# Kernel tuning notes

Hardware: AMD Instinct MI355X
Metric: run time of the kernel (lower is better)

## Reference

```python
import jax, jax.numpy as jnp
import numpy as np

N = 100000      # nodes
E = 1_000_000   # edges (avg degree ~10)
D_IN = 64
HID = 64
N_CLS = 32


def setup_inputs() -> dict:
    key = jax.random.key(0)
    ks = jax.random.split(key, 9)
    x = jax.random.normal(ks[0], (N, D_IN), dtype=jnp.float32)
    edge_index = jax.random.randint(ks[1], (2, E), 0, N, dtype=jnp.int32)
    s_in = 1.0 / np.sqrt(D_IN)
    s_h = 1.0 / np.sqrt(HID)
    W1 = jax.random.normal(ks[2], (D_IN, HID), dtype=jnp.float32) * s_in
    b1 = jnp.zeros((HID,), dtype=jnp.float32)
    W2 = jax.random.normal(ks[3], (HID, HID), dtype=jnp.float32) * s_h
    b2 = jnp.zeros((HID,), dtype=jnp.float32)
    Wl = jax.random.normal(ks[4], (HID, N_CLS), dtype=jnp.float32) * s_h
    bl = jnp.zeros((N_CLS,), dtype=jnp.float32)
    return {"x": x, "edge_index": edge_index,
            "W1": W1, "b1": b1, "W2": W2, "b2": b2, "Wl": Wl, "bl": bl}


def reference(x, edge_index, W1, b1, W2, b2, Wl, bl):
    # GCNConv default: add self-loops, symmetric normalization D^-1/2 (A+I) D^-1/2
    loop = jnp.arange(N, dtype=edge_index.dtype)
    src = jnp.concatenate([edge_index[0], loop])  # [E+N]
    dst = jnp.concatenate([edge_index[1], loop])  # [E+N]

    deg = jax.ops.segment_sum(jnp.ones_like(dst, dtype=jnp.float32), dst,
                              num_segments=N)              # [N]
    dinv = jnp.where(deg > 0, jax.lax.rsqrt(deg), 0.0)      # D^-1/2
    norm = dinv[src] * dinv[dst]                            # [E+N]

    def gcn_conv(h, W, b):
        h = h @ W                                           # [N, F_out]
        msg = h[src] * norm[:, None]                        # gather + scale
        return jax.ops.segment_sum(msg, dst, num_segments=N) + b

    h = jax.nn.relu(gcn_conv(x, W1, b1))
    h = jax.nn.relu(gcn_conv(h, W2, b2))
    return h @ Wl + bl
```

## Files before the change

### kernel.cpp

```cpp
#include <hip/hip_runtime.h>
#include <hip/hip_fp16.h>
#include <math.h>


#define TPB    256
#define TPB1   1024
#define EBLKS  256
#define BSH    7
#define BNODES (1 << BSH)

__global__ __launch_bounds__(TPB1)
void k_p1hist(const int* __restrict__ dst, int* __restrict__ OFS,
              int E, int CH, int NBC) {
    __shared__ int h[1024];
    int tid = threadIdx.x, b = blockIdx.x;
    h[tid] = 0;
    __syncthreads();
    int beg = b * CH, end = min(E, beg + CH);
    if (beg < end) {
        int nfull = (end - beg) & ~3;
        for (int i = beg + tid * 4; i < beg + nfull; i += TPB1 * 4) {
            int4 d = *(const int4*)&dst[i];
            atomicAdd(&h[d.x >> BSH], 1);
            atomicAdd(&h[d.y >> BSH], 1);
            atomicAdd(&h[d.z >> BSH], 1);
            atomicAdd(&h[d.w >> BSH], 1);
        }
        if (tid < (end - beg) - nfull)
            atomicAdd(&h[dst[beg + nfull + tid] >> BSH], 1);
    }
    __syncthreads();
    for (int c = tid; c < NBC; c += TPB1) OFS[c * EBLKS + b] = h[c];
}

__global__ __launch_bounds__(TPB)
void k_scanA(const int* __restrict__ OFS, int* __restrict__ bsum, int total) {
    __shared__ int s[TPB];
    int tid = threadIdx.x;
    int i0  = blockIdx.x * 1024 + tid * 4;
    int t = 0;
#pragma unroll
    for (int k = 0; k < 4; ++k) {
        int i = i0 + k;
        t += (i < total) ? OFS[i] : 0;
    }
    s[tid] = t;
    __syncthreads();
    for (int off = TPB / 2; off > 0; off >>= 1) {
        if (tid < off) s[tid] += s[tid + off];
        __syncthreads();
    }
    if (tid == 0) bsum[blockIdx.x] = s[0];
}

__global__ __launch_bounds__(TPB)
void k_scanC(int* __restrict__ OFS, const int* __restrict__ bsum, int total) {
    __shared__ int s[TPB];
    __shared__ int pfx;
    int tid = threadIdx.x;
    if (tid < 64) {
        int v = 0;
        for (int j = tid; j < (int)blockIdx.x; j += 64) v += bsum[j];
#pragma unroll
        for (int off = 1; off < 64; off <<= 1) v += __shfl_xor(v, off);
        if (tid == 0) pfx = v;
    }
    int i0 = blockIdx.x * 1024 + tid * 4;
    int v[4];
#pragma unroll
    for (int k = 0; k < 4; ++k) {
        int i = i0 + k;
        v[k] = (i < total) ? OFS[i] : 0;
    }
    int tsum = v[0] + v[1] + v[2] + v[3];
    s[tid] = tsum;
    __syncthreads();
    for (int off = 1; off < TPB; off <<= 1) {
        int x = (tid >= off) ? s[tid - off] : 0;
        __syncthreads();
        s[tid] += x;
        __syncthreads();
    }
    int base = pfx + (s[tid] - tsum);
#pragma unroll
    for (int k = 0; k < 4; ++k) {
        int i = i0 + k;
        if (i < total) {
            OFS[i] = base;
            base += v[k];
        }
    }
}

__global__ __launch_bounds__(TPB1)
void k_p1scatter(const int* __restrict__ src, const int* __restrict__ dst,
                 const int* __restrict__ OFS, int* __restrict__ ebuf,
                 int E, int CH, int NBC) {
    __shared__ int cur[1024];
    int tid = threadIdx.x, b = blockIdx.x;
    for (int c = tid; c < NBC; c += TPB1) cur[c] = OFS[c * EBLKS + b];
    __syncthreads();
    int beg = b * CH, end = min(E, beg + CH);
    if (beg >= end) return;
    int nfull = (end - beg) & ~3;
    for (int i = beg + tid * 4; i < beg + nfull; i += TPB1 * 4) {
        int4 s4 = *(const int4*)&src[i];
        int4 d4 = *(const int4*)&dst[i];
        int p0 = atomicAdd(&cur[d4.x >> BSH], 1);
        int p1 = atomicAdd(&cur[d4.y >> BSH], 1);
        int p2 = atomicAdd(&cur[d4.z >> BSH], 1);
        int p3 = atomicAdd(&cur[d4.w >> BSH], 1);
        ebuf[p0] = (s4.x << BSH) | (d4.x & (BNODES - 1));
        ebuf[p1] = (s4.y << BSH) | (d4.y & (BNODES - 1));
        ebuf[p2] = (s4.z << BSH) | (d4.z & (BNODES - 1));
        ebuf[p3] = (s4.w << BSH) | (d4.w & (BNODES - 1));
    }
    if (tid < (end - beg) - nfull) {
        int i = beg + nfull + tid;
        int d = dst[i];
        int p = atomicAdd(&cur[d >> BSH], 1);
        ebuf[p] = (src[i] << BSH) | (d & (BNODES - 1));
    }
}

__global__ __launch_bounds__(TPB)
void k_p2(const int* __restrict__ ebuf, const int* __restrict__ OFS,
          int* __restrict__ row_ptr, float* __restrict__ dinv,
          int* __restrict__ colw, int N, int E, int NBC) {
    __shared__ int cnt[BNODES];
    __shared__ int ofs[BNODES];
    __shared__ int s1[TPB];
    int tid = threadIdx.x, c = blockIdx.x;
    int beg = OFS[c * EBLKS];
    int end = (c == NBC - 1) ? E : OFS[(c + 1) * EBLKS];
    if (tid < BNODES) cnt[tid] = 0;
    __syncthreads();
    for (int i = beg + tid; i < end; i += TPB)
        atomicAdd(&cnt[ebuf[i] & (BNODES - 1)], 1);
    __syncthreads();
    int a = (tid < BNODES) ? cnt[tid] : 0;
    s1[tid] = a;
    __syncthreads();
    for (int off = 1; off < TPB; off <<= 1) {
        int x = (tid >= off) ? s1[tid - off] : 0;
        __syncthreads();
        s1[tid] += x;
        __syncthreads();
    }
    int ex = s1[tid] - a;
    if (tid < BNODES) {
        int node = (c << BSH) + tid;
        ofs[tid] = beg + ex;
        if (node < N) {
            row_ptr[node] = beg + ex;
            dinv[node]    = rsqrtf((float)(a + 1));
        }
        cnt[tid] = 0;
    }
    if (c == NBC - 1 && tid == 0) row_ptr[N] = E;
    __syncthreads();
    for (int i0 = beg + tid; i0 < end; i0 += TPB * 4) {
        int sv[4], dl[4], pos[4];
        int have = 0;
#pragma unroll
        for (int k = 0; k < 4; ++k) {
            int i = i0 + k * TPB;
            if (i < end) {
                int e = ebuf[i];
                sv[k] = e >> BSH;
                dl[k] = e & (BNODES - 1);
                have = k + 1;
            }
        }
#pragma unroll
        for (int k = 0; k < 4; ++k) {
            if (k < have) {
                int r  = atomicAdd(&cnt[dl[k]], 1);
                pos[k] = ofs[dl[k]] + r;
            }
        }
#pragma unroll
        for (int k = 0; k < 4; ++k)
            if (k < have) colw[pos[k]] = sv[k];
    }
}

__launch_bounds__(256)
__global__ void k_mm(const float* __restrict__ in, const float* __restrict__ W,
                     const float* __restrict__ dinv,
                     __half* __restrict__ out, int n) {
    __shared__ float in_s[64 * 68];
    __shared__ float w_s[64 * 64];

    const int tid  = threadIdx.x;
    const int row0 = blockIdx.x * 64;

    for (int i4 = tid; i4 < (64 * 64) / 4; i4 += 256)
        ((float4*)w_s)[i4] = ((const float4*)W)[i4];

    for (int idx = tid; idx < 64 * 16; idx += 256) {
        int r  = idx >> 4;
        int c4 = idx & 15;
        float4 v;
        if (row0 + r < n)
            v = *(const float4*)(in + (size_t)(row0 + r) * 64 + c4 * 4);
        else
            v = make_float4(0.f, 0.f, 0.f, 0.f);
        *(float4*)&in_s[r * 68 + c4 * 4] = v;
    }
    __syncthreads();

    constexpr int CPT = 4;
    const int tx = tid & 15;
    const int ty = tid >> 4;

    float acc[4][CPT];
#pragma unroll
    for (int r = 0; r < 4; ++r)
#pragma unroll
        for (int c = 0; c < CPT; ++c) acc[r][c] = 0.f;

#pragma unroll 4
    for (int k = 0; k < 64; ++k) {
        float b[CPT];
#pragma unroll
        for (int c = 0; c < CPT; ++c) b[c] = w_s[k * 64 + tx * CPT + c];
#pragma unroll
        for (int r = 0; r < 4; ++r) {
            float a = in_s[(ty * 4 + r) * 68 + k];
#pragma unroll
            for (int c = 0; c < CPT; ++c) acc[r][c] = fmaf(a, b[c], acc[r][c]);
        }
    }

#pragma unroll
    for (int r = 0; r < 4; ++r) {
        int row = row0 + ty * 4 + r;
        if (row >= n) continue;
        float dd = dinv[row];
        __half2 p0 = __floats2half2_rn(acc[r][0] * dd, acc[r][1] * dd);
        __half2 p1 = __floats2half2_rn(acc[r][2] * dd, acc[r][3] * dd);
        uint2 u = make_uint2(*(unsigned*)&p0, *(unsigned*)&p1);
        *(uint2*)(out + (size_t)row * 64 + tx * 4) = u;
    }
    if (blockIdx.x == 0 && tid < 16)
        *(uint2*)(out + (size_t)n * 64 + tid * 4) = make_uint2(0u, 0u);
}

__global__ __launch_bounds__(256)
void k_gather_mm(const int* __restrict__ row_ptr, const int* __restrict__ colw,
                 const float* __restrict__ dinv, const float* __restrict__ bias,
                 const __half* __restrict__ t, const float* __restrict__ W2,
                 __half* __restrict__ t2, int N) {
    __shared__ float  w_s[64 * 64];
    __shared__ __half aggs[32][72];

    int tid = threadIdx.x;
    for (int i4 = tid; i4 < (64 * 64) / 4; i4 += 256)
        ((float4*)w_s)[i4] = ((const float4*)W2)[i4];

    int wv   = tid >> 6;
    int lane = tid & 63;
    int g = lane >> 3;
    int p = lane & 7;
    int slot = tid >> 3;
    int d = blockIdx.x * 32 + wv * 8 + g;

    int beg = 0, end = 0;
    if (d < N) { beg = row_ptr[d]; end = row_ptr[d + 1]; }

    float acc[8];
#pragma unroll
    for (int k = 0; k < 8; ++k) acc[k] = 0.f;

    for (int e = beg; e < end; e += 4) {
        int s0 = colw[e];
        int s1 = (e + 1 < end) ? colw[e + 1] : N;
        int s2 = (e + 2 < end) ? colw[e + 2] : N;
        int s3 = (e + 3 < end) ? colw[e + 3] : N;
        uint4 a0 = *(const uint4*)(t + (size_t)s0 * 64 + p * 8);
        uint4 a1 = *(const uint4*)(t + (size_t)s1 * 64 + p * 8);
        uint4 a2 = *(const uint4*)(t + (size_t)s2 * 64 + p * 8);
        uint4 a3 = *(const uint4*)(t + (size_t)s3 * 64 + p * 8);
        float2 f;
        f = __half22float2(*(__half2*)&a0.x); acc[0] += f.x; acc[1] += f.y;
        f = __half22float2(*(__half2*)&a0.y); acc[2] += f.x; acc[3] += f.y;
        f = __half22float2(*(__half2*)&a0.z); acc[4] += f.x; acc[5] += f.y;
        f = __half22float2(*(__half2*)&a0.w); acc[6] += f.x; acc[7] += f.y;
        f = __half22float2(*(__half2*)&a1.x); acc[0] += f.x; acc[1] += f.y;
        f = __half22float2(*(__half2*)&a1.y); acc[2] += f.x; acc[3] += f.y;
        f = __half22float2(*(__half2*)&a1.z); acc[4] += f.x; acc[5] += f.y;
        f = __half22float2(*(__half2*)&a1.w); acc[6] += f.x; acc[7] += f.y;
        f = __half22float2(*(__half2*)&a2.x); acc[0] += f.x; acc[1] += f.y;
        f = __half22float2(*(__half2*)&a2.y); acc[2] += f.x; acc[3] += f.y;
        f = __half22float2(*(__half2*)&a2.z); acc[4] += f.x; acc[5] += f.y;
        f = __half22float2(*(__half2*)&a2.w); acc[6] += f.x; acc[7] += f.y;
        f = __half22float2(*(__half2*)&a3.x); acc[0] += f.x; acc[1] += f.y;
        f = __half22float2(*(__half2*)&a3.y); acc[2] += f.x; acc[3] += f.y;
        f = __half22float2(*(__half2*)&a3.z); acc[4] += f.x; acc[5] += f.y;
        f = __half22float2(*(__half2*)&a3.w); acc[6] += f.x; acc[7] += f.y;
    }

    if (d < N) {
        float dd = dinv[d];
        uint4 a = *(const uint4*)(t + (size_t)d * 64 + p * 8);
        float4 b0 = *(const float4*)&bias[p * 8];
        float4 b1 = *(const float4*)&bias[p * 8 + 4];
        float2 s0 = __half22float2(*(__half2*)&a.x);
        float2 s1 = __half22float2(*(__half2*)&a.y);
        float2 s2 = __half22float2(*(__half2*)&a.z);
        float2 s3 = __half22float2(*(__half2*)&a.w);
        float o0 = fmaxf(fmaf(dd, acc[0] + s0.x, b0.x), 0.f);
        float o1 = fmaxf(fmaf(dd, acc[1] + s0.y, b0.y), 0.f);
        float o2 = fmaxf(fmaf(dd, acc[2] + s1.x, b0.z), 0.f);
        float o3 = fmaxf(fmaf(dd, acc[3] + s1.y, b0.w), 0.f);
        float o4 = fmaxf(fmaf(dd, acc[4] + s2.x, b1.x), 0.f);
        float o5 = fmaxf(fmaf(dd, acc[5] + s2.y, b1.y), 0.f);
        float o6 = fmaxf(fmaf(dd, acc[6] + s3.x, b1.z), 0.f);
        float o7 = fmaxf(fmaf(dd, acc[7] + s3.y, b1.w), 0.f);
        __half2 h0 = __floats2half2_rn(o0, o1);
        __half2 h1 = __floats2half2_rn(o2, o3);
        __half2 h2 = __floats2half2_rn(o4, o5);
        __half2 h3 = __floats2half2_rn(o6, o7);
        *(uint4*)&aggs[slot][p * 8] = make_uint4(*(unsigned*)&h0, *(unsigned*)&h1,
                                                *(unsigned*)&h2, *(unsigned*)&h3);
    }
    __syncthreads();

    if (d < N) {
        float dd = dinv[d];
        float a0 = 0.f, a1 = 0.f, a2 = 0.f, a3 = 0.f;
        float a4 = 0.f, a5 = 0.f, a6 = 0.f, a7 = 0.f;
#pragma unroll
        for (int k0 = 0; k0 < 64; k0 += 8) {
            uint4 u = *(const uint4*)&aggs[slot][k0];
            float2 f0 = __half22float2(*(__half2*)&u.x);
            float2 f1 = __half22float2(*(__half2*)&u.y);
            float2 f2 = __half22float2(*(__half2*)&u.z);
            float2 f3 = __half22float2(*(__half2*)&u.w);
            float av[8] = {f0.x, f0.y, f1.x, f1.y, f2.x, f2.y, f3.x, f3.y};
#pragma unroll
            for (int j = 0; j < 8; ++j) {
                const float* wr = &w_s[(k0 + j) * 64 + p * 8];
                float4 w0 = *(const float4*)&wr[0];
                float4 w1 = *(const float4*)&wr[4];
                a0 = fmaf(av[j], w0.x, a0);
                a1 = fmaf(av[j], w0.y, a1);
                a2 = fmaf(av[j], w0.z, a2);
                a3 = fmaf(av[j], w0.w, a3);
                a4 = fmaf(av[j], w1.x, a4);
                a5 = fmaf(av[j], w1.y, a5);
                a6 = fmaf(av[j], w1.z, a6);
                a7 = fmaf(av[j], w1.w, a7);
            }
        }
        __half2 q0 = __floats2half2_rn(a0 * dd, a1 * dd);
        __half2 q1 = __floats2half2_rn(a2 * dd, a3 * dd);
        __half2 q2 = __floats2half2_rn(a4 * dd, a5 * dd);
        __half2 q3 = __floats2half2_rn(a6 * dd, a7 * dd);
        uint4 u = make_uint4(*(unsigned*)&q0, *(unsigned*)&q1,
                             *(unsigned*)&q2, *(unsigned*)&q3);
        *(uint4*)(t2 + (size_t)d * 64 + p * 8) = u;
    }
    if (blockIdx.x == 0 && tid < 16)
        *(uint2*)(t2 + (size_t)N * 64 + tid * 4) = make_uint2(0u, 0u);
}

__global__ __launch_bounds__(256)
void k_gather_head(const int* __restrict__ row_ptr, const int* __restrict__ colw,
                   const float* __restrict__ dinv, const float* __restrict__ bias,
                   const __half* __restrict__ t, const float* __restrict__ Wl,
                   const float* __restrict__ bl, float* __restrict__ out, int N) {
    __shared__ float wl_s[64 * 32];
    __shared__ float aggs[32][68];

    int tid  = threadIdx.x;
    for (int i4 = tid; i4 < (64 * 32) / 4; i4 += 256)
        ((float4*)wl_s)[i4] = ((const float4*)Wl)[i4];

    int wv   = tid >> 6;
    int lane = tid & 63;
    int g = lane >> 3;
    int p = lane & 7;
    int slot = tid >> 3;
    int d = blockIdx.x * 32 + wv * 8 + g;

    int beg = 0, end = 0;
    if (d < N) { beg = row_ptr[d]; end = row_ptr[d + 1]; }

    float acc[8];
#pragma unroll
    for (int k = 0; k < 8; ++k) acc[k] = 0.f;

    for (int e = beg; e < end; e += 4) {
        int s0 = colw[e];
        int s1 = (e + 1 < end) ? colw[e + 1] : N;
        int s2 = (e + 2 < end) ? colw[e + 2] : N;
        int s3 = (e + 3 < end) ? colw[e + 3] : N;
        uint4 a0 = *(const uint4*)(t + (size_t)s0 * 64 + p * 8);
        uint4 a1 = *(const uint4*)(t + (size_t)s1 * 64 + p * 8);
        uint4 a2 = *(const uint4*)(t + (size_t)s2 * 64 + p * 8);
        uint4 a3 = *(const uint4*)(t + (size_t)s3 * 64 + p * 8);
        float2 f;
        f = __half22float2(*(__half2*)&a0.x); acc[0] += f.x; acc[1] += f.y;
        f = __half22float2(*(__half2*)&a0.y); acc[2] += f.x; acc[3] += f.y;
        f = __half22float2(*(__half2*)&a0.z); acc[4] += f.x; acc[5] += f.y;
        f = __half22float2(*(__half2*)&a0.w); acc[6] += f.x; acc[7] += f.y;
        f = __half22float2(*(__half2*)&a1.x); acc[0] += f.x; acc[1] += f.y;
        f = __half22float2(*(__half2*)&a1.y); acc[2] += f.x; acc[3] += f.y;
        f = __half22float2(*(__half2*)&a1.z); acc[4] += f.x; acc[5] += f.y;
        f = __half22float2(*(__half2*)&a1.w); acc[6] += f.x; acc[7] += f.y;
        f = __half22float2(*(__half2*)&a2.x); acc[0] += f.x; acc[1] += f.y;
        f = __half22float2(*(__half2*)&a2.y); acc[2] += f.x; acc[3] += f.y;
        f = __half22float2(*(__half2*)&a2.z); acc[4] += f.x; acc[5] += f.y;
        f = __half22float2(*(__half2*)&a2.w); acc[6] += f.x; acc[7] += f.y;
        f = __half22float2(*(__half2*)&a3.x); acc[0] += f.x; acc[1] += f.y;
        f = __half22float2(*(__half2*)&a3.y); acc[2] += f.x; acc[3] += f.y;
        f = __half22float2(*(__half2*)&a3.z); acc[4] += f.x; acc[5] += f.y;
        f = __half22float2(*(__half2*)&a3.w); acc[6] += f.x; acc[7] += f.y;
    }

    if (d < N) {
        float dd = dinv[d];
        uint4 a = *(const uint4*)(t + (size_t)d * 64 + p * 8);
        float4 b0 = *(const float4*)&bias[p * 8];
        float4 b1 = *(const float4*)&bias[p * 8 + 4];
        float2 s0 = __half22float2(*(__half2*)&a.x);
        float2 s1 = __half22float2(*(__half2*)&a.y);
        float2 s2 = __half22float2(*(__half2*)&a.z);
        float2 s3 = __half22float2(*(__half2*)&a.w);
        float o0 = fmaxf(fmaf(dd, acc[0] + s0.x, b0.x), 0.f);
        float o1 = fmaxf(fmaf(dd, acc[1] + s0.y, b0.y), 0.f);
        float o2 = fmaxf(fmaf(dd, acc[2] + s1.x, b0.z), 0.f);
        float o3 = fmaxf(fmaf(dd, acc[3] + s1.y, b0.w), 0.f);
        float o4 = fmaxf(fmaf(dd, acc[4] + s2.x, b1.x), 0.f);
        float o5 = fmaxf(fmaf(dd, acc[5] + s2.y, b1.y), 0.f);
        float o6 = fmaxf(fmaf(dd, acc[6] + s3.x, b1.z), 0.f);
        float o7 = fmaxf(fmaf(dd, acc[7] + s3.y, b1.w), 0.f);
        *(float4*)&aggs[slot][p * 8]     = make_float4(o0, o1, o2, o3);
        *(float4*)&aggs[slot][p * 8 + 4] = make_float4(o4, o5, o6, o7);
    }
    __syncthreads();

    if (d < N) {
        float a0 = 0.f, a1 = 0.f, a2 = 0.f, a3 = 0.f;
#pragma unroll 8
        for (int k = 0; k < 64; ++k) {
            float av = aggs[slot][k];
            float4 w = ((const float4*)&wl_s[k * 32])[p];
            a0 = fmaf(av, w.x, a0);
            a1 = fmaf(av, w.y, a1);
            a2 = fmaf(av, w.z, a2);
            a3 = fmaf(av, w.w, a3);
        }
        float4 bb = *(const float4*)&bl[p * 4];
        *(float4*)&out[(size_t)d * 32 + p * 4] =
            make_float4(a0 + bb.x, a1 + bb.y, a2 + bb.z, a3 + bb.w);
    }
}

extern "C" void kernel_launch(void* const* d_in, const int* in_sizes, int n_in,
                              void* d_out, int out_size, void* d_ws, size_t ws_size,
                              hipStream_t stream) {
    const float* x  = (const float*)d_in[0];
    const int*   ei = (const int*)d_in[1];
    const float* W1 = (const float*)d_in[2];
    const float* b1 = (const float*)d_in[3];
    const float* W2 = (const float*)d_in[4];
    const float* b2 = (const float*)d_in[5];
    const float* Wl = (const float*)d_in[6];
    const float* bl = (const float*)d_in[7];
    float*       out = (float*)d_out;

    const int N = in_sizes[0] / 64;
    const int E = in_sizes[1] / 2;
    const int* srcp = ei;
    const int* dstp = ei + E;

    const int NBC   = (N + BNODES - 1) / BNODES;
    const int CH    = (((E + EBLKS - 1) / EBLKS) + 3) & ~3;
    const int total = NBC * EBLKS;
    const int NBLK  = (total + 1023) / 1024;

    char*  ws  = (char*)d_ws;
    size_t off = 0;
    auto alloc = [&](size_t bytes) -> void* {
        void* p = (void*)(ws + off);
        off += (bytes + 255) & ~(size_t)255;
        return p;
    };
    int*    OFS     = (int*)alloc(((size_t)total + 1) * 4);
    int*    bsum    = (int*)alloc((size_t)NBLK * 4);
    int*    ebuf    = (int*)alloc((size_t)E * 4);
    int*    row_ptr = (int*)alloc((size_t)(N + 1) * 4);
    float*  dinv    = (float*)alloc((size_t)N * 4);
    int*    colw    = (int*)alloc((size_t)E * 4);
    __half* t1      = (__half*)alloc((size_t)(N + 1) * 64 * 2);
    __half* t2      = (__half*)alloc((size_t)(N + 1) * 64 * 2);

    const int nb_mm = (N + 63) / 64;
    const int nb_g  = (N + 31) / 32;

    k_p1hist   <<<EBLKS, TPB1, 0, stream>>>(dstp, OFS, E, CH, NBC);
    k_scanA    <<<NBLK,  TPB,  0, stream>>>(OFS, bsum, total);
    k_scanC    <<<NBLK,  TPB,  0, stream>>>(OFS, bsum, total);
    k_p1scatter<<<EBLKS, TPB1, 0, stream>>>(srcp, dstp, OFS, ebuf, E, CH, NBC);
    k_p2       <<<NBC,   TPB,  0, stream>>>(ebuf, OFS, row_ptr, dinv, colw, N, E, NBC);

    k_mm<<<nb_mm, 256, 0, stream>>>(x, W1, dinv, t1, N);

    k_gather_mm<<<nb_g, 256, 0, stream>>>(row_ptr, colw, dinv, b1, t1,
                                          W2, t2, N);

    k_gather_head<<<nb_g, 256, 0, stream>>>(row_ptr, colw, dinv, b2, t2,
                                            Wl, bl, out, N);
}
```

Before: 187.1 us.

## Fuse scan into single pass and merge CSR build with first matmul

The two-kernel scan (block sums, then prefix) is replaced by one kernel in which each block re-reads and sums all preceding OFS entries itself, writing to a separate OFS2 buffer to avoid read/write races. The per-bucket CSR build kernel now also performs the x@W1 matmul for its 128 nodes, using the dinv values it already holds in shared memory. This removes two kernel launches and a global dinv re-read. In exchange the scan does redundant reads that grow with block index, and the fused kernel uses more shared memory, which may lower occupancy.

```diff
diff --git a/kernel.cpp b/kernel.cpp
--- a/kernel.cpp
+++ b/kernel.cpp
@@ -34,38 +34,27 @@
 }
 
 __global__ __launch_bounds__(TPB)
-void k_scanA(const int* __restrict__ OFS, int* __restrict__ bsum, int total) {
+void k_scan1(const int* __restrict__ OFS, int* __restrict__ OFS2, int total) {
     __shared__ int s[TPB];
+    __shared__ int pfxs;
     int tid = threadIdx.x;
-    int i0  = blockIdx.x * 1024 + tid * 4;
-    int t = 0;
-#pragma unroll
-    for (int k = 0; k < 4; ++k) {
-        int i = i0 + k;
-        t += (i < total) ? OFS[i] : 0;
-    }
-    s[tid] = t;
+    int lim = blockIdx.x * 1024;
+
+    int acc = 0;
+    for (int i = tid * 4; i < lim; i += TPB * 4) {
+        int4 v = *(const int4*)&OFS[i];
+        acc += v.x + v.y + v.z + v.w;
+    }
+    s[tid] = acc;
     __syncthreads();
     for (int off = TPB / 2; off > 0; off >>= 1) {
         if (tid < off) s[tid] += s[tid + off];
         __syncthreads();
     }
-    if (tid == 0) bsum[blockIdx.x] = s[0];
-}
-
-__global__ __launch_bounds__(TPB)
-void k_scanC(int* __restrict__ OFS, const int* __restrict__ bsum, int total) {
-    __shared__ int s[TPB];
-    __shared__ int pfx;
-    int tid = threadIdx.x;
-    if (tid < 64) {
-        int v = 0;
-        for (int j = tid; j < (int)blockIdx.x; j += 64) v += bsum[j];
-#pragma unroll
-        for (int off = 1; off < 64; off <<= 1) v += __shfl_xor(v, off);
-        if (tid == 0) pfx = v;
-    }
-    int i0 = blockIdx.x * 1024 + tid * 4;
+    if (tid == 0) pfxs = s[0];
+    __syncthreads();
+
+    int i0 = lim + tid * 4;
     int v[4];
 #pragma unroll
     for (int k = 0; k < 4; ++k) {
@@ -81,12 +70,12 @@
         s[tid] += x;
         __syncthreads();
     }
-    int base = pfx + (s[tid] - tsum);
+    int base = pfxs + (s[tid] - tsum);
 #pragma unroll
     for (int k = 0; k < 4; ++k) {
         int i = i0 + k;
         if (i < total) {
-            OFS[i] = base;
+            OFS2[i] = base;
             base += v[k];
         }
     }
@@ -94,11 +83,11 @@
 
 __global__ __launch_bounds__(TPB1)
 void k_p1scatter(const int* __restrict__ src, const int* __restrict__ dst,
-                 const int* __restrict__ OFS, int* __restrict__ ebuf,
+                 const int* __restrict__ OFS2, int* __restrict__ ebuf,
                  int E, int CH, int NBC) {
     __shared__ int cur[1024];
     int tid = threadIdx.x, b = blockIdx.x;
-    for (int c = tid; c < NBC; c += TPB1) cur[c] = OFS[c * EBLKS + b];
+    for (int c = tid; c < NBC; c += TPB1) cur[c] = OFS2[c * EBLKS + b];
     __syncthreads();
     int beg = b * CH, end = min(E, beg + CH);
     if (beg >= end) return;
@@ -124,15 +113,25 @@
 }
 
 __global__ __launch_bounds__(TPB)
-void k_p2(const int* __restrict__ ebuf, const int* __restrict__ OFS,
-          int* __restrict__ row_ptr, float* __restrict__ dinv,
-          int* __restrict__ colw, int N, int E, int NBC) {
-    __shared__ int cnt[BNODES];
-    __shared__ int ofs[BNODES];
-    __shared__ int s1[TPB];
+void k_p2mm(const int* __restrict__ ebuf, const int* __restrict__ OFS2,
+            const float* __restrict__ x, const float* __restrict__ W1,
+            int* __restrict__ row_ptr, float* __restrict__ dinv,
+            int* __restrict__ colw, __half* __restrict__ t1,
+            int N, int E, int NBC) {
+    __shared__ int   cnt[BNODES];
+    __shared__ int   ofs[BNODES];
+    __shared__ int   s1[TPB];
+    __shared__ float dinv_s[BNODES];
+    __shared__ float in_s[64 * 68];
+    __shared__ float w_s[64 * 64];
+
     int tid = threadIdx.x, c = blockIdx.x;
-    int beg = OFS[c * EBLKS];
-    int end = (c == NBC - 1) ? E : OFS[(c + 1) * EBLKS];
+
+    for (int i4 = tid; i4 < (64 * 64) / 4; i4 += TPB)
+        ((float4*)w_s)[i4] = ((const float4*)W1)[i4];
+
+    int beg = OFS2[c * EBLKS];
+    int end = (c == NBC - 1) ? E : OFS2[(c + 1) * EBLKS];
     if (tid < BNODES) cnt[tid] = 0;
     __syncthreads();
     for (int i = beg + tid; i < end; i += TPB)
@@ -142,18 +141,20 @@
     s1[tid] = a;
     __syncthreads();
     for (int off = 1; off < TPB; off <<= 1) {
-        int x = (tid >= off) ? s1[tid - off] : 0;
-        __syncthreads();
-        s1[tid] += x;
+        int v = (tid >= off) ? s1[tid - off] : 0;
+        __syncthreads();
+        s1[tid] += v;
         __syncthreads();
     }
     int ex = s1[tid] - a;
     if (tid < BNODES) {
         int node = (c << BSH) + tid;
-        ofs[tid] = beg + ex;
+        float dv = rsqrtf((float)(a + 1));
+        ofs[tid]    = beg + ex;
+        dinv_s[tid] = dv;
         if (node < N) {
             row_ptr[node] = beg + ex;
-            dinv[node]    = rsqrtf((float)(a + 1));
+            dinv[node]    = dv;
         }
         cnt[tid] = 0;
     }
@@ -183,68 +184,57 @@
         for (int k = 0; k < 4; ++k)
             if (k < have) colw[pos[k]] = sv[k];
     }
-}
-
-__launch_bounds__(256)
-__global__ void k_mm(const float* __restrict__ in, const float* __restrict__ W,
-                     const float* __restrict__ dinv,
-                     __half* __restrict__ out, int n) {
-    __shared__ float in_s[64 * 68];
-    __shared__ float w_s[64 * 64];
-
-    const int tid  = threadIdx.x;
-    const int row0 = blockIdx.x * 64;
-
-    for (int i4 = tid; i4 < (64 * 64) / 4; i4 += 256)
-        ((float4*)w_s)[i4] = ((const float4*)W)[i4];
-
-    for (int idx = tid; idx < 64 * 16; idx += 256) {
-        int r  = idx >> 4;
-        int c4 = idx & 15;
-        float4 v;
-        if (row0 + r < n)
-            v = *(const float4*)(in + (size_t)(row0 + r) * 64 + c4 * 4);
-        else
-            v = make_float4(0.f, 0.f, 0.f, 0.f);
-        *(float4*)&in_s[r * 68 + c4 * 4] = v;
-    }
-    __syncthreads();
-
-    constexpr int CPT = 4;
+
     const int tx = tid & 15;
     const int ty = tid >> 4;
-
-    float acc[4][CPT];
-#pragma unroll
-    for (int r = 0; r < 4; ++r)
-#pragma unroll
-        for (int c = 0; c < CPT; ++c) acc[r][c] = 0.f;
+#pragma unroll
+    for (int half = 0; half < 2; ++half) {
+        const int row0 = (c << BSH) + half * 64;
+        __syncthreads();
+        for (int idx = tid; idx < 64 * 16; idx += TPB) {
+            int r  = idx >> 4;
+            int c4 = idx & 15;
+            float4 v = make_float4(0.f, 0.f, 0.f, 0.f);
+            if (row0 + r < N)
+                v = *(const float4*)(x + (size_t)(row0 + r) * 64 + c4 * 4);
+            *(float4*)&in_s[r * 68 + c4 * 4] = v;
+        }
+        __syncthreads();
+
+        float acc[4][4];
+#pragma unroll
+        for (int r = 0; r < 4; ++r)
+#pragma unroll
+            for (int cc = 0; cc < 4; ++cc) acc[r][cc] = 0.f;
 
 #pragma unroll 4
-    for (int k = 0; k < 64; ++k) {
-        float b[CPT];
-#pragma unroll
-        for (int c = 0; c < CPT; ++c) b[c] = w_s[k * 64 + tx * CPT + c];
+        for (int k = 0; k < 64; ++k) {
+            float b[4];
+#pragma unroll
+            for (int cc = 0; cc < 4; ++cc) b[cc] = w_s[k * 64 + tx * 4 + cc];
+#pragma unroll
+            for (int r = 0; r < 4; ++r) {
+                float av = in_s[(ty * 4 + r) * 68 + k];
+#pragma unroll
+                for (int cc = 0; cc < 4; ++cc)
+                    acc[r][cc] = fmaf(av, b[cc], acc[r][cc]);
+            }
+        }
+
 #pragma unroll
         for (int r = 0; r < 4; ++r) {
-            float a = in_s[(ty * 4 + r) * 68 + k];
-#pragma unroll
-            for (int c = 0; c < CPT; ++c) acc[r][c] = fmaf(a, b[c], acc[r][c]);
-        }
-    }
-
-#pragma unroll
-    for (int r = 0; r < 4; ++r) {
-        int row = row0 + ty * 4 + r;
-        if (row >= n) continue;
-        float dd = dinv[row];
-        __half2 p0 = __floats2half2_rn(acc[r][0] * dd, acc[r][1] * dd);
-        __half2 p1 = __floats2half2_rn(acc[r][2] * dd, acc[r][3] * dd);
-        uint2 u = make_uint2(*(unsigned*)&p0, *(unsigned*)&p1);
-        *(uint2*)(out + (size_t)row * 64 + tx * 4) = u;
-    }
-    if (blockIdx.x == 0 && tid < 16)
-        *(uint2*)(out + (size_t)n * 64 + tid * 4) = make_uint2(0u, 0u);
+            int lrow = ty * 4 + r;
+            int row  = row0 + lrow;
+            if (row >= N) continue;
+            float dd = dinv_s[half * 64 + lrow];
+            __half2 p0 = __floats2half2_rn(acc[r][0] * dd, acc[r][1] * dd);
+            __half2 p1 = __floats2half2_rn(acc[r][2] * dd, acc[r][3] * dd);
+            uint2 u = make_uint2(*(unsigned*)&p0, *(unsigned*)&p1);
+            *(uint2*)(t1 + (size_t)row * 64 + tx * 4) = u;
+        }
+    }
+    if (c == 0 && tid < 16)
+        *(uint2*)(t1 + (size_t)N * 64 + tid * 4) = make_uint2(0u, 0u);
 }
 
 __global__ __launch_bounds__(256)
@@ -490,7 +480,7 @@
         return p;
     };
     int*    OFS     = (int*)alloc(((size_t)total + 1) * 4);
-    int*    bsum    = (int*)alloc((size_t)NBLK * 4);
+    int*    OFS2    = (int*)alloc(((size_t)total + 1) * 4);
     int*    ebuf    = (int*)alloc((size_t)E * 4);
     int*    row_ptr = (int*)alloc((size_t)(N + 1) * 4);
     float*  dinv    = (float*)alloc((size_t)N * 4);
@@ -498,16 +488,14 @@
     __half* t1      = (__half*)alloc((size_t)(N + 1) * 64 * 2);
     __half* t2      = (__half*)alloc((size_t)(N + 1) * 64 * 2);
 
-    const int nb_mm = (N + 63) / 64;
     const int nb_g  = (N + 31) / 32;
 
     k_p1hist   <<<EBLKS, TPB1, 0, stream>>>(dstp, OFS, E, CH, NBC);
-    k_scanA    <<<NBLK,  TPB,  0, stream>>>(OFS, bsum, total);
-    k_scanC    <<<NBLK,  TPB,  0, stream>>>(OFS, bsum, total);
-    k_p1scatter<<<EBLKS, TPB1, 0, stream>>>(srcp, dstp, OFS, ebuf, E, CH, NBC);
-    k_p2       <<<NBC,   TPB,  0, stream>>>(ebuf, OFS, row_ptr, dinv, colw, N, E, NBC);
-
-    k_mm<<<nb_mm, 256, 0, stream>>>(x, W1, dinv, t1, N);
+    k_scan1    <<<NBLK,  TPB,  0, stream>>>(OFS, OFS2, total);
+    k_p1scatter<<<EBLKS, TPB1, 0, stream>>>(srcp, dstp, OFS2, ebuf, E, CH, NBC);
+
+    k_p2mm<<<NBC, TPB, 0, stream>>>(ebuf, OFS2, x, W1, row_ptr, dinv, colw,
+                                    t1, N, E, NBC);
 
     k_gather_mm<<<nb_g, 256, 0, stream>>>(row_ptr, colw, dinv, b1, t1,
                                           W2, t2, N);
```

Measured after the change: 208.9 us. 1.12x slower.
